# Optimization experiments

Measured on AMD Instinct MI355X. Metric: run time of the kernel, lower is better.

The kernel has to match this reference:

```python
import jax, jax.numpy as jnp
import numpy as np
from jax import lax
import math

N_QUBITS = 10
N_LAYERS = 4
PI = jnp.float32(math.pi)


def _c(x):
    return x.astype(jnp.complex64)


def rx_mat(t):
    c = _c(jnp.cos(0.5 * t)); s = _c(jnp.sin(0.5 * t))
    return jnp.stack([jnp.stack([c, -1j * s]), jnp.stack([-1j * s, c])])


def ry_mat(t):
    c = _c(jnp.cos(0.5 * t)); s = _c(jnp.sin(0.5 * t))
    return jnp.stack([jnp.stack([c, -s]), jnp.stack([s, c])])


def rz_mat(t):
    e0 = jnp.exp(_c(jnp.zeros_like(t)) - 0.5j * _c(t))
    e1 = jnp.exp(0.5j * _c(t))
    z = jnp.zeros_like(e0)
    return jnp.stack([jnp.stack([e0, z]), jnp.stack([z, e1])])


def apply_1q(psi, U, q):
    # psi: (2,)*n complex, apply 2x2 U on axis q
    psi = jnp.moveaxis(psi, q, 0)
    psi = jnp.tensordot(U, psi, axes=(1, 0))
    return jnp.moveaxis(psi, 0, q)


def apply_cnot(psi, ctrl, tgt):
    psi = jnp.moveaxis(psi, (ctrl, tgt), (0, 1))
    a00, a01, a10, a11 = psi[0, 0], psi[0, 1], psi[1, 0], psi[1, 1]
    psi = jnp.stack([jnp.stack([a00, a01]), jnp.stack([a11, a10])])
    return jnp.moveaxis(psi, (0, 1), (ctrl, tgt))


def vqc(state, weights):
    # state: (D,) float32 angles; weights: (layers, n, 3)
    n, L = N_QUBITS, N_LAYERS
    D = state.shape[0]
    psi = jnp.full((2,) * n, 2.0 ** (-n / 2.0), dtype=jnp.complex64)  # H^n |0>
    for layer in range(L):
        for q in range(n):
            ang = state[(layer * n + q) % D]
            psi = apply_1q(psi, rx_mat(ang), q)
            psi = apply_1q(psi, ry_mat(ang), q)
            psi = apply_1q(psi, rz_mat(weights[layer, q, 0]), q)
            psi = apply_1q(psi, ry_mat(weights[layer, q, 1]), q)
            psi = apply_1q(psi, rz_mat(weights[layer, q, 2]), q)
        for q in range(n - 1):
            psi = apply_cnot(psi, q, q + 1)
        psi = apply_cnot(psi, n - 1, 0)
    probs = jnp.real(psi * jnp.conj(psi))  # (2,)*n
    zdiag = jnp.array([1.0, -1.0], dtype=jnp.float32)
    exps = [jnp.sum(probs * zdiag.reshape((1,) * q + (2,) + (1,) * (n - q - 1)))
            for q in range(n)]
    return jnp.stack(exps)  # (n,)


def lstm_forward(x, W_ih, W_hh, b_ih, b_hh):
    # x: [B,T,Din]; PyTorch gate order: i, f, g, o
    B, T, _ = x.shape
    H = W_hh.shape[1]
    b = b_ih + b_hh

    def step(carry, xt):
        h, c = carry
        gates = xt @ W_ih.T + h @ W_hh.T + b
        i, f, g, o = jnp.split(gates, 4, axis=-1)
        i = jax.nn.sigmoid(i); f = jax.nn.sigmoid(f)
        g = jnp.tanh(g); o = jax.nn.sigmoid(o)
        c = f * c + i * g
        h = o * jnp.tanh(c)
        return (h, c), h

    h0 = jnp.zeros((B, H), x.dtype)
    c0 = jnp.zeros((B, H), x.dtype)
    _, hs = lax.scan(step, (h0, c0), jnp.swapaxes(x, 0, 1))
    return jnp.swapaxes(hs, 0, 1)  # [B,T,H]


def _forward(s, lstm_s, W_ih, W_hh, b_ih, b_hh, proj_W, proj_b,
             in_proj_W, in_proj_b, out_proj_W, out_proj_b,
             qweights, W1, b1, W2, b2):
    hs = lstm_forward(lstm_s, W_ih, W_hh, b_ih, b_hh)      # [B,T,H]
    lstm_last = hs[:, -1, :]                               # [B,H]
    state_full = jnp.concatenate([lstm_last, s], axis=1)   # [B,E]
    lstm_proj = hs @ proj_W.T + proj_b                     # [B,T,E]
    E = proj_W.shape[0]
    Wq, Wk, Wv = in_proj_W[:E], in_proj_W[E:2 * E], in_proj_W[2 * E:]
    bq, bk, bv = in_proj_b[:E], in_proj_b[E:2 * E], in_proj_b[2 * E:]
    q = state_full @ Wq.T + bq                             # [B,E] (1 query token)
    k = lstm_proj @ Wk.T + bk                              # [B,T,E]
    v = lstm_proj @ Wv.T + bv
    scale = 1.0 / jnp.sqrt(jnp.float32(E))                 # num_heads=1 -> head_dim=E
    attn = jax.nn.softmax(jnp.einsum('be,bte->bt', q, k) * scale, axis=-1)
    ctx = jnp.einsum('bt,bte->be', attn, v)
    attn_out = ctx @ out_proj_W.T + out_proj_b             # [B,E]
    merged_state = jnp.concatenate([attn_out, s], axis=1)  # [B,E+F]
    state_norm = jnp.tanh(merged_state) * PI
    qfeat = jax.vmap(lambda st: vqc(st, qweights))(state_norm)  # [B,n]
    merged = jnp.concatenate([merged_state, qfeat], axis=1)
    x = jax.nn.relu(merged @ W1.T + b1)
    return x @ W2.T + b2


def setup_inputs() -> dict:
    key = jax.random.key(0)
    ks = jax.random.split(key, 16)
    B, T = 512, 256
    Din, H, F = 128, 256, 64
    E = H + F          # 320 = state_dim
    Dm = E + F         # 384 = merged_state dim
    n_l1, n_act = 512, 8

    def g(k, shape, std):
        return (std * jax.random.normal(k, shape)).astype(jnp.float32)

    return {
        's': jax.random.normal(ks[0], (B, F), jnp.float32),
        'lstm_s': jax.random.normal(ks[1], (B, T, Din), jnp.float32),
        'W_ih': g(ks[2], (4 * H, Din), 0.05),
        'W_hh': g(ks[3], (4 * H, H), 0.05),
        'b_ih': jnp.zeros((4 * H,), jnp.float32),
        'b_hh': jnp.zeros((4 * H,), jnp.float32),
        'proj_W': g(ks[4], (E, H), 0.05),
        'proj_b': 0.1 * jnp.ones((E,), jnp.float32),
        'in_proj_W': g(ks[5], (3 * E, E), 0.05),
        'in_proj_b': jnp.zeros((3 * E,), jnp.float32),
        'out_proj_W': g(ks[6], (E, E), 0.05),
        'out_proj_b': jnp.zeros((E,), jnp.float32),
        'qweights': jax.random.uniform(ks[7], (N_LAYERS, N_QUBITS, 3), jnp.float32, 0.0, 2.0 * math.pi),
        'W1': g(ks[8], (n_l1, Dm + N_QUBITS), 0.05),
        'b1': 0.1 * jnp.ones((n_l1,), jnp.float32),
        'W2': g(ks[9], (n_act, n_l1), 0.05),
        'b2': 0.1 * jnp.ones((n_act,), jnp.float32),
    }


def reference(s, lstm_s, W_ih, W_hh, b_ih, b_hh, proj_W, proj_b,
              in_proj_W, in_proj_b, out_proj_W, out_proj_b,
              qweights, W1, b1, W2, b2):
    return _forward(s, lstm_s, W_ih, W_hh, b_ih, b_hh, proj_W, proj_b,
                    in_proj_W, in_proj_b, out_proj_W, out_proj_b,
                    qweights, W1, b1, W2, b2)
```

## Files before the change

### kernel.cpp

```cpp
#include <hip/hip_runtime.h>
#include <hip/hip_bf16.h>
#include <math.h>

typedef unsigned int u32;
typedef unsigned long long u64;
typedef unsigned short u16;
typedef __attribute__((ext_vector_type(8))) short short8;
typedef __attribute__((ext_vector_type(4))) float f32x4;
typedef __attribute__((ext_vector_type(4))) int v4i;

#define PI_F 3.14159265358979f
#define B_   512
#define T_   256
#define DIN  128
#define H_   256
#define G4   1024
#define F_   64
#define E_   320
#define DM   384
#define NL1  512
#define NACT 8
#define KMLP 394

__device__ v4i llvm_amdgcn_raw_buffer_load_v4i32(v4i rsrc, int voffset,
                                                 int soffset, int aux)
    __asm("llvm.amdgcn.raw.buffer.load.v4i32");
__device__ void llvm_amdgcn_raw_buffer_store_i32(int vdata, v4i rsrc,
                                                 int voffset, int soffset,
                                                 int aux)
    __asm("llvm.amdgcn.raw.buffer.store.i32");

__device__ __forceinline__ v4i make_srd(const void* p) {
  v4i r;
  r.x = (int)(u32)(u64)p;
  r.y = (int)(u32)((u64)p >> 32);
  r.z = (int)0xFFFFFFFFu;
  r.w = 0x00020000;
  return r;
}

__device__ __forceinline__ float b2f(u16 h) {
  union { u32 u; float f; } v; v.u = ((u32)h) << 16; return v.f;
}
__device__ __forceinline__ u16 f2b(float f) {
  union { float f; u32 u; } v; v.f = f;
  u32 r = (v.u + 0x7FFFu + ((v.u >> 16) & 1u)) >> 16;
  return (u16)r;
}
__device__ __forceinline__ float sigf(float x) { return 1.0f / (1.0f + __expf(-x)); }
__device__ __forceinline__ float tanhfast(float x) { return 2.0f / (1.0f + __expf(-2.0f * x)) - 1.0f; }
__device__ __forceinline__ float2 cmul(float2 a, float2 b) {
  return make_float2(a.x * b.x - a.y * b.y, a.x * b.y + a.y * b.x);
}
__device__ __forceinline__ float2 cadd(float2 a, float2 b) {
  return make_float2(a.x + b.x, a.y + b.y);
}

__global__ void k_prep1(const float* __restrict__ lstm_s,
                        const float* __restrict__ W_ih,
                        const float* __restrict__ W_hh,
                        const float* __restrict__ b_ih,
                        const float* __restrict__ b_hh,
                        const float* __restrict__ ipw,
                        const float* __restrict__ ipb,
                        const float* __restrict__ projb,
                        const float* __restrict__ qw,
                        const float* __restrict__ W1,
                        u16* __restrict__ xbf,
                        u16* __restrict__ hs,
                        u16* __restrict__ Wg,
                        float* __restrict__ bb,
                        float* __restrict__ W1t,
                        float* __restrict__ uw,
                        float* __restrict__ bkp,
                        float* __restrict__ bvp,
                        u32* __restrict__ cnt) {
  const int bid = blockIdx.x;
  const int tid = threadIdx.x;
  if (bid < 8192) {
    u32 u = (u32)bid * 256u + tid;
    u32 c8 = u & 15u, b = (u >> 4) & 511u, t = u >> 13;
    const float* src = lstm_s + ((size_t)b * T_ + t) * DIN + c8 * 8;
    union { u16 h[8]; uint4 v; } tmp;
#pragma unroll
    for (int i = 0; i < 8; ++i) tmp.h[i] = f2b(src[i]);
    *(uint4*)(xbf + ((size_t)t * B_ + b) * DIN + c8 * 8) = tmp.v;
  } else if (bid < 8384) {
    u32 u = (u32)(bid - 8192) * 256u + tid;
    u32 c8 = u % 48u, r = u / 48u;
    const float* src = (c8 < 16) ? (W_ih + (size_t)r * DIN + c8 * 8)
                                 : (W_hh + (size_t)r * H_ + (c8 - 16) * 8);
    union { u16 h[8]; uint4 v; } tmp;
#pragma unroll
    for (int i = 0; i < 8; ++i) tmp.h[i] = f2b(src[i]);
    *(uint4*)(Wg + (size_t)r * 384 + c8 * 8) = tmp.v;
  } else if (bid < 8448) {
    u32 u = (u32)(bid - 8384) * 256u + tid;
    ((uint4*)hs)[u] = make_uint4(0, 0, 0, 0);
  } else if (bid < 9236) {
    u32 u = (u32)(bid - 8448) * 256u + tid;
    u32 k = u / 512u, nn = u % 512u;
    W1t[u] = W1[(size_t)nn * KMLP + k];
  } else if (bid == 9236) {
    for (int i = tid; i < 1024; i += 256) bb[i] = b_ih[i] + b_hh[i];
    for (int i = tid; i < 1024; i += 256) cnt[i] = 0u;
    if (tid < 40) {
      float w0 = qw[tid * 3 + 0], w1 = qw[tid * 3 + 1], w2 = qw[tid * 3 + 2];
      float c0 = cosf(0.5f * w0), s0 = sinf(0.5f * w0);
      float c1 = cosf(0.5f * w1), s1 = sinf(0.5f * w1);
      float c2 = cosf(0.5f * w2), s2 = sinf(0.5f * w2);
      float2 e0m = make_float2(c0, -s0), e0p = make_float2(c0, s0);
      float2 e2m = make_float2(c2, -s2), e2p = make_float2(c2, s2);
      float2 t00 = make_float2(c1 * e0m.x, c1 * e0m.y);
      float2 t01 = make_float2(-s1 * e0p.x, -s1 * e0p.y);
      float2 t10 = make_float2(s1 * e0m.x, s1 * e0m.y);
      float2 t11 = make_float2(c1 * e0p.x, c1 * e0p.y);
      float2 u00 = cmul(e2m, t00), u01 = cmul(e2m, t01);
      float2 u10 = cmul(e2p, t10), u11 = cmul(e2p, t11);
      float* o = uw + tid * 8;
      o[0] = u00.x; o[1] = u00.y; o[2] = u01.x; o[3] = u01.y;
      o[4] = u10.x; o[5] = u10.y; o[6] = u11.x; o[7] = u11.y;
    }
  } else if (bid <= 9238) {
    int o = (bid - 9237) * 256 + tid;
    if (o < E_) {
      float acc = ipb[E_ + o];
      for (int e = 0; e < E_; ++e) acc += ipw[(size_t)(E_ + o) * E_ + e] * projb[e];
      bkp[o] = acc;
    }
  } else {
    int o = (bid - 9239) * 256 + tid;
    if (o < E_) {
      float acc = ipb[2 * E_ + o];
      for (int e = 0; e < E_; ++e) acc += ipw[(size_t)(2 * E_ + o) * E_ + e] * projb[e];
      bvp[o] = acc;
    }
  }
}

__global__ void k_prep2(const float* __restrict__ ipw, const float* __restrict__ projW,
                        float* __restrict__ Wkp, float* __restrict__ Wvp) {
  int bid = blockIdx.x, tid = threadIdx.x;
  int o = (bid < 320) ? bid : (bid - 320);
  const float* wrow = ipw + (size_t)((bid < 320 ? E_ : 2 * E_) + o) * E_;
  float acc = 0.f;
  for (int e = 0; e < E_; ++e) acc += wrow[e] * projW[(size_t)e * H_ + tid];
  (bid < 320 ? Wkp : Wvp)[(size_t)o * H_ + tid] = acc;
}

__global__ void k_prep3(const float* __restrict__ ipw, const float* __restrict__ ipb,
                        const float* __restrict__ opw, const float* __restrict__ opb,
                        const float* __restrict__ Wkp, const float* __restrict__ Wvp,
                        const float* __restrict__ bkp, const float* __restrict__ bvp,
                        float* __restrict__ WuT, float* __restrict__ bu,
                        float* __restrict__ wd, float* __restrict__ ddp,
                        float* __restrict__ Wovt, float* __restrict__ bov) {
  int bid = blockIdx.x, tid = threadIdx.x;
  if (bid < 320) {
    int e = bid;
    float acc = 0.f;
    for (int o = 0; o < E_; ++o) acc += Wkp[(size_t)o * H_ + tid] * ipw[(size_t)o * E_ + e];
    WuT[(size_t)e * H_ + tid] = acc;
  } else if (bid < 576) {
    int jj = bid - 320;
    for (int i = tid; i < E_; i += 256) {
      float acc = 0.f;
      for (int o = 0; o < E_; ++o) acc += opw[(size_t)i * E_ + o] * Wvp[(size_t)o * H_ + jj];
      Wovt[(size_t)jj * E_ + i] = acc;
    }
  } else {
    {
      float acc = 0.f;
      for (int o = 0; o < E_; ++o) acc += Wkp[(size_t)o * H_ + tid] * ipb[o];
      bu[tid] = acc;
    }
    for (int idx = tid; idx < E_; idx += 256) {
      float a1 = 0.f, a2 = opb[idx];
      for (int o = 0; o < E_; ++o) {
        a1 += ipw[(size_t)o * E_ + idx] * bkp[o];
        a2 += opw[(size_t)idx * E_ + o] * bvp[o];
      }
      wd[idx] = a1; bov[idx] = a2;
    }
    if (tid == 0) {
      float acc = 0.f;
      for (int o = 0; o < E_; ++o) acc += ipb[o] * bkp[o];
      ddp[0] = acc;
    }
  }
}

struct LstmArgs {
  const u16* xbf; u16* hs; const u16* Wg; const float* bb; u32* cnt;
};

__launch_bounds__(256, 1)
__global__ void k_lstm(LstmArgs A) {
  const int g   = blockIdx.x & 7;
  const int n   = blockIdx.x >> 3;
  const int tid = threadIdx.x;
  const int wid = tid >> 6, lane = tid & 63;
  __shared__ __align__(16) u16 Wl[32 * 392];

  for (int idx = tid; idx < 32 * 48; idx += 256) {
    int ln = idx / 48, c8 = idx % 48;
    int gr = (ln >> 3) * 256 + n * 8 + (ln & 7);
    *(uint4*)&Wl[ln * 392 + c8 * 8] = *(const uint4*)&A.Wg[(size_t)gr * 384 + c8 * 8];
  }
  const int j  = lane & 7;
  const int gc = n * 8 + j;
  const float bbi = A.bb[gc], bbf2 = A.bb[256 + gc];
  const float bbg = A.bb[512 + gc], bbo = A.bb[768 + gc];

  const int quad = lane >> 4;
  const int mrow = lane & 15;
  const int brow = g * 64 + wid * 16 + mrow;
  const int erow0 = g * 64 + wid * 16 + quad * 4;
  const bool hi = (lane & 8) != 0;
  float crs[4] = {0.f, 0.f, 0.f, 0.f};
  u32* mycnt = A.cnt + g * 64;
  u32 target = 0;

  const v4i hs_srd = make_srd(A.hs);
  const int hvoff = (brow * H_ + quad * 8) * 2;

  uint4 xc0, xc1, xc2, xc3, xn0, xn1, xn2, xn3;
  {
    const u16* xb = A.xbf + ((size_t)0 * B_ + brow) * DIN + quad * 8;
    xc0 = *(const uint4*)(xb + 0);
    xc1 = *(const uint4*)(xb + 32);
    xc2 = *(const uint4*)(xb + 64);
    xc3 = *(const uint4*)(xb + 96);
  }
  __syncthreads();

  for (int t = 0; t < T_; ++t) {
    const int hsoff = t * (B_ * H_ * 2);
    uint4 h0 = __builtin_bit_cast(uint4, llvm_amdgcn_raw_buffer_load_v4i32(hs_srd, hvoff +   0, hsoff, 17));
    uint4 h1 = __builtin_bit_cast(uint4, llvm_amdgcn_raw_buffer_load_v4i32(hs_srd, hvoff +  64, hsoff, 17));
    uint4 h2 = __builtin_bit_cast(uint4, llvm_amdgcn_raw_buffer_load_v4i32(hs_srd, hvoff + 128, hsoff, 17));
    uint4 h3 = __builtin_bit_cast(uint4, llvm_amdgcn_raw_buffer_load_v4i32(hs_srd, hvoff + 192, hsoff, 17));
    uint4 h4 = __builtin_bit_cast(uint4, llvm_amdgcn_raw_buffer_load_v4i32(hs_srd, hvoff + 256, hsoff, 17));
    uint4 h5 = __builtin_bit_cast(uint4, llvm_amdgcn_raw_buffer_load_v4i32(hs_srd, hvoff + 320, hsoff, 17));
    uint4 h6 = __builtin_bit_cast(uint4, llvm_amdgcn_raw_buffer_load_v4i32(hs_srd, hvoff + 384, hsoff, 17));
    uint4 h7 = __builtin_bit_cast(uint4, llvm_amdgcn_raw_buffer_load_v4i32(hs_srd, hvoff + 448, hsoff, 17));
    {
      const int tn = (t + 1 < T_) ? (t + 1) : t;
      const u16* xb = A.xbf + ((size_t)tn * B_ + brow) * DIN + quad * 8;
      xn0 = *(const uint4*)(xb + 0);
      xn1 = *(const uint4*)(xb + 32);
      xn2 = *(const uint4*)(xb + 64);
      xn3 = *(const uint4*)(xb + 96);
    }

    f32x4 acc0 = {0.f, 0.f, 0.f, 0.f}, acc1 = {0.f, 0.f, 0.f, 0.f};
#define MMSTEP(AV, KOFF)                                                          \
    {                                                                             \
      short8 av  = __builtin_bit_cast(short8, AV);                                \
      short8 bv0 = __builtin_bit_cast(short8,                                     \
          *(const uint4*)&Wl[mrow * 392 + (KOFF) + quad * 8]);                    \
      short8 bv1 = __builtin_bit_cast(short8,                                     \
          *(const uint4*)&Wl[(16 + mrow) * 392 + (KOFF) + quad * 8]);             \
      acc0 = __builtin_amdgcn_mfma_f32_16x16x32_bf16(av, bv0, acc0, 0, 0, 0);     \
      acc1 = __builtin_amdgcn_mfma_f32_16x16x32_bf16(av, bv1, acc1, 0, 0, 0);     \
    }
    MMSTEP(xc0, 0)   MMSTEP(xc1, 32)  MMSTEP(xc2, 64)  MMSTEP(xc3, 96)
    MMSTEP(h0, 128)  MMSTEP(h1, 160)  MMSTEP(h2, 192)  MMSTEP(h3, 224)
    MMSTEP(h4, 256)  MMSTEP(h5, 288)  MMSTEP(h6, 320)  MMSTEP(h7, 352)
#undef MMSTEP

    const int hsoff_o = (t + 1) * (B_ * H_ * 2);
#pragma unroll
    for (int r = 0; r < 4; ++r) {
      float x0 = acc0[r], x1v = acc1[r];
      float y0 = __shfl_xor(x0, 8, 64);
      float y1 = __shfl_xor(x1v, 8, 64);
      float iv = (hi ? y0 : x0) + bbi;
      float fv = (hi ? x0 : y0) + bbf2;
      float gv = (hi ? y1 : x1v) + bbg;
      float ov = (hi ? x1v : y1) + bbo;
      float cc = sigf(fv) * crs[r] + sigf(iv) * tanhfast(gv);
      crs[r] = cc;
      float hh = sigf(ov) * tanhfast(cc);
      float hh2 = __shfl_xor(hh, 1, 64);
      if (!hi && ((j & 1) == 0)) {
        u32 pk = (u32)f2b(hh) | ((u32)f2b(hh2) << 16);
        llvm_amdgcn_raw_buffer_store_i32((int)pk, hs_srd,
                                         ((erow0 + r) * H_ + gc) * 2, hsoff_o, 17);
      }
    }
    target += 32;
    if (t != T_ - 1) {
      __syncthreads();
      if (tid == 0) {
        __hip_atomic_fetch_add(mycnt, 1u, __ATOMIC_RELAXED, __HIP_MEMORY_SCOPE_AGENT);
        int guard = 0;
        while (__hip_atomic_load(mycnt, __ATOMIC_RELAXED, __HIP_MEMORY_SCOPE_AGENT) < target) {
          __builtin_amdgcn_s_sleep(1);
          if (++guard > (1 << 24)) break;
        }
      }
      __syncthreads();
      xc0 = xn0; xc1 = xn1; xc2 = xn2; xc3 = xn3;
    }
  }
}

__global__ void k_post(const u16* __restrict__ hs, const float* __restrict__ s,
                       const float* __restrict__ WuT, const float* __restrict__ bu,
                       const float* __restrict__ wd, const float* __restrict__ ddp,
                       const float* __restrict__ Wovt, const float* __restrict__ bov,
                       const float* __restrict__ uwg,
                       const float* __restrict__ W1t, const float* __restrict__ b1,
                       const float* __restrict__ W2, const float* __restrict__ b2,
                       float* __restrict__ out) {
  int b = blockIdx.x, tid = threadIdx.x;
  int wid = tid >> 6, lane = tid & 63;
  __shared__ float z[E_];
  __shared__ float red[256];
  __shared__ float ul_s[H_];
  __shared__ float sc[T_];
  __shared__ float wv_s[H_];
  __shared__ float mst_l[DM];
  __shared__ float dvec_s;
  __shared__ float2 psi[1024];
  __shared__ float ang[40];
  __shared__ float uwl[320];
  __shared__ float part[4][10];
  __shared__ float qf_s[10];
  __shared__ float mg[KMLP];
  __shared__ float x1[NL1];

  z[tid] = b2f(hs[((size_t)T_ * B_ + b) * H_ + tid]);
  if (tid < F_) z[H_ + tid] = s[(size_t)b * F_ + tid];
  __syncthreads();
  {
    float acc = bu[tid];
    for (int e = 0; e < E_; ++e) acc += WuT[(size_t)e * H_ + tid] * z[e];
    ul_s[tid] = acc;
    float p = 0.f;
    for (int e = tid; e < E_; e += 256) p += wd[e] * z[e];
    red[tid] = p;
    __syncthreads();
    for (int s2 = 128; s2 > 0; s2 >>= 1) {
      if (tid < s2) red[tid] += red[tid + s2];
      __syncthreads();
    }
    if (tid == 0) dvec_s = red[0] + ddp[0];
    __syncthreads();
  }

  {
    const float db = dvec_s;
    const float scale = 0.055901699437494745f;
    float4 ul = make_float4(ul_s[lane * 4], ul_s[lane * 4 + 1],
                            ul_s[lane * 4 + 2], ul_s[lane * 4 + 3]);
    for (int tt = 0; tt < 64; ++tt) {
      int t = wid * 64 + tt;
      u32 rw0 = ((const u32*)(hs + ((size_t)(t + 1) * B_ + b) * H_))[lane * 2];
      u32 rw1 = ((const u32*)(hs + ((size_t)(t + 1) * B_ + b) * H_))[lane * 2 + 1];
      union { u32 uu; float f; } f0, f1, f2, f3;
      f0.uu = rw0 << 16; f1.uu = rw0 & 0xFFFF0000u;
      f2.uu = rw1 << 16; f3.uu = rw1 & 0xFFFF0000u;
      float p = f0.f * ul.x + f1.f * ul.y + f2.f * ul.z + f3.f * ul.w;
#pragma unroll
      for (int off = 32; off > 0; off >>= 1) p += __shfl_xor(p, off, 64);
      if (lane == 0) sc[t] = (p + db) * scale;
    }
    __syncthreads();
    float v = sc[tid];
    red[tid] = v;
    __syncthreads();
    for (int s2 = 128; s2 > 0; s2 >>= 1) {
      if (tid < s2) red[tid] = fmaxf(red[tid], red[tid + s2]);
      __syncthreads();
    }
    float m = red[0];
    __syncthreads();
    float e = __expf(v - m);
    red[tid] = e;
    __syncthreads();
    for (int s2 = 128; s2 > 0; s2 >>= 1) {
      if (tid < s2) red[tid] += red[tid + s2];
      __syncthreads();
    }
    float inv = 1.f / red[0];
    __syncthreads();
    sc[tid] = e * inv;
    __syncthreads();
    float acc = 0.f;
#pragma unroll 8
    for (int t = 0; t < T_; ++t) {
      acc += sc[t] * b2f(hs[((size_t)(t + 1) * B_ + b) * H_ + tid]);
    }
    wv_s[tid] = acc;
    __syncthreads();
  }

  {
    for (int i = tid; i < E_; i += 256) {
      float acc = bov[i];
      for (int jj = 0; jj < H_; ++jj) acc += Wovt[(size_t)jj * E_ + i] * wv_s[jj];
      mst_l[i] = acc;
    }
    if (tid < F_) mst_l[E_ + tid] = s[(size_t)b * F_ + tid];
    __syncthreads();
  }

  {
    if (tid < 40) ang[tid] = tanhf(mst_l[tid]) * PI_F;
    uwl[tid] = uwg[tid];
    if (tid < 64) uwl[256 + tid] = uwg[256 + tid];
#pragma unroll
    for (int k = 0; k < 4; ++k) psi[tid + k * 256] = make_float2(0.03125f, 0.f);
    __syncthreads();
    for (int l = 0; l < 4; ++l) {
      for (int q = 0; q < 10; ++q) {
        int lq = l * 10 + q;
        float a = ang[lq];
        float ca = __cosf(0.5f * a), sa = __sinf(0.5f * a);
        float cs = ca * sa;
        float2 m00 = make_float2(ca * ca, sa * sa);
        float2 m01 = make_float2(-cs, -cs);
        float2 m10 = make_float2(cs, -cs);
        float2 m11 = make_float2(ca * ca, -sa * sa);
        const float* uwp = &uwl[lq * 8];
        float2 a00 = make_float2(uwp[0], uwp[1]), a01 = make_float2(uwp[2], uwp[3]);
        float2 a10 = make_float2(uwp[4], uwp[5]), a11 = make_float2(uwp[6], uwp[7]);
        float2 u00 = cadd(cmul(a00, m00), cmul(a01, m10));
        float2 u01 = cadd(cmul(a00, m01), cmul(a01, m11));
        float2 u10 = cadd(cmul(a10, m00), cmul(a11, m10));
        float2 u11 = cadd(cmul(a10, m01), cmul(a11, m11));
        int bp = 9 - q;
        __syncthreads();
#pragma unroll
        for (int k = 0; k < 2; ++k) {
          int p = tid + k * 256;
          int i0 = ((p >> bp) << (bp + 1)) | (p & ((1 << bp) - 1));
          int i1 = i0 | (1 << bp);
          float2 A0 = psi[i0], A1 = psi[i1];
          psi[i0] = cadd(cmul(u00, A0), cmul(u01, A1));
          psi[i1] = cadd(cmul(u10, A0), cmul(u11, A1));
        }
      }
      for (int q = 0; q < 9; ++q) {
        int lo = 8 - q;
        __syncthreads();
        int p = tid;
        int i0 = ((p >> lo) << (lo + 2)) | (2 << lo) | (p & ((1 << lo) - 1));
        int i1 = i0 | (1 << lo);
        float2 tmp = psi[i0]; psi[i0] = psi[i1]; psi[i1] = tmp;
      }
      __syncthreads();
      {
        int i0 = (tid << 1) | 1;
        int i1 = i0 | 512;
        float2 tmp = psi[i0]; psi[i0] = psi[i1]; psi[i1] = tmp;
      }
    }
    __syncthreads();
    float acc[10];
#pragma unroll
    for (int q = 0; q < 10; ++q) acc[q] = 0.f;
#pragma unroll
    for (int k = 0; k < 4; ++k) {
      int idx = tid + k * 256;
      float2 A = psi[idx];
      float pr = A.x * A.x + A.y * A.y;
#pragma unroll
      for (int q = 0; q < 10; ++q) acc[q] += ((idx >> (9 - q)) & 1) ? -pr : pr;
    }
#pragma unroll
    for (int q = 0; q < 10; ++q) {
      float vq = acc[q];
#pragma unroll
      for (int off = 32; off > 0; off >>= 1) vq += __shfl_xor(vq, off, 64);
      if (lane == 0) part[wid][q] = vq;
    }
    __syncthreads();
    if (tid < 10) qf_s[tid] = part[0][tid] + part[1][tid] + part[2][tid] + part[3][tid];
  }

  {
    for (int i = tid; i < DM; i += 256) mg[i] = mst_l[i];
    if (tid < 10) mg[DM + tid] = qf_s[tid];
    __syncthreads();
#pragma unroll
    for (int hh = 0; hh < 2; ++hh) {
      int nn = tid + hh * 256;
      float acc = b1[nn];
#pragma unroll 4
      for (int k = 0; k < KMLP; ++k) acc += W1t[(size_t)k * NL1 + nn] * mg[k];
      x1[nn] = fmaxf(acc, 0.f);
    }
    __syncthreads();
    int a = tid >> 5, l32 = tid & 31;
    float p = 0.f;
    for (int k = l32; k < NL1; k += 32) p += x1[k] * W2[(size_t)a * NL1 + k];
    red[tid] = p;
    __syncthreads();
    if (tid < 8) {
      float acc = b2[tid];
#pragma unroll
      for (int i = 0; i < 32; ++i) acc += red[tid * 32 + i];
      out[(size_t)b * NACT + tid] = acc;
    }
  }
}

extern "C" void kernel_launch(void* const* d_in, const int* in_sizes, int n_in,
                              void* d_out, int out_size, void* d_ws, size_t ws_size,
                              hipStream_t stream) {
  const float* s      = (const float*)d_in[0];
  const float* lstm_s = (const float*)d_in[1];
  const float* W_ih   = (const float*)d_in[2];
  const float* W_hh   = (const float*)d_in[3];
  const float* b_ih   = (const float*)d_in[4];
  const float* b_hh   = (const float*)d_in[5];
  const float* projW  = (const float*)d_in[6];
  const float* projb  = (const float*)d_in[7];
  const float* ipw    = (const float*)d_in[8];
  const float* ipb    = (const float*)d_in[9];
  const float* opw    = (const float*)d_in[10];
  const float* opb    = (const float*)d_in[11];
  const float* qw     = (const float*)d_in[12];
  const float* W1     = (const float*)d_in[13];
  const float* b1     = (const float*)d_in[14];
  const float* W2     = (const float*)d_in[15];
  const float* b2     = (const float*)d_in[16];
  float* out = (float*)d_out;

  char* wsb = (char*)d_ws;
  size_t off = 0;
  auto alloc = [&](size_t bytes) -> void* {
    void* p = wsb + off;
    off = (off + bytes + 255) & ~(size_t)255;
    return p;
  };
  u16*  xbf  = (u16*)alloc((size_t)T_ * B_ * DIN * 2);
  u16*  hs   = (u16*)alloc((size_t)(T_ + 1) * B_ * H_ * 2);
  u16*  Wg   = (u16*)alloc((size_t)G4 * 384 * 2);
  float* bb  = (float*)alloc(G4 * 4);
  float* Wkp = (float*)alloc((size_t)E_ * H_ * 4);
  float* Wvp = (float*)alloc((size_t)E_ * H_ * 4);
  float* bkp = (float*)alloc(E_ * 4);
  float* bvp = (float*)alloc(E_ * 4);
  float* WuT = (float*)alloc((size_t)E_ * H_ * 4);
  float* bu  = (float*)alloc(H_ * 4);
  float* wd  = (float*)alloc(E_ * 4);
  float* ddp = (float*)alloc(256);
  float* Wovt= (float*)alloc((size_t)H_ * E_ * 4);
  float* bov = (float*)alloc(E_ * 4);
  float* uw  = (float*)alloc(40 * 8 * 4);
  float* W1t = (float*)alloc((size_t)KMLP * NL1 * 4);
  u32*  cnt  = (u32*)alloc(1024 * 4);
  (void)ws_size; (void)in_sizes; (void)n_in; (void)out_size;

  hipLaunchKernelGGL(k_prep1, dim3(9241), dim3(256), 0, stream,
                     lstm_s, W_ih, W_hh, b_ih, b_hh, ipw, ipb, projb, qw, W1,
                     xbf, hs, Wg, bb, W1t, uw, bkp, bvp, cnt);
  hipLaunchKernelGGL(k_prep2, dim3(640), dim3(256), 0, stream, ipw, projW, Wkp, Wvp);
  hipLaunchKernelGGL(k_prep3, dim3(577), dim3(256), 0, stream,
                     ipw, ipb, opw, opb, Wkp, Wvp, bkp, bvp, WuT, bu, wd, ddp, Wovt, bov);

  LstmArgs la;
  la.xbf = xbf; la.hs = hs; la.Wg = Wg; la.bb = bb; la.cnt = cnt;
  void* kargs[] = { (void*)&la };
  hipError_t ce = hipLaunchCooperativeKernel(reinterpret_cast<const void*>(&k_lstm),
                                             dim3(256), dim3(256), kargs, 0, stream);
  if (ce != hipSuccess) {
    hipLaunchKernelGGL(k_lstm, dim3(256), dim3(256), 0, stream, la);
  }

  hipLaunchKernelGGL(k_post, dim3(512), dim3(256), 0, stream,
                     hs, s, WuT, bu, wd, ddp, Wovt, bov, uw, W1t, b1, W2, b2, out);
}
```

Before: 1.295 ms.

## Fold attention weight precompute into extra LSTM blocks and split post accumulators

```diff
diff --git a/kernel.cpp b/kernel.cpp
--- a/kernel.cpp
+++ b/kernel.cpp
@@ -25,10 +25,17 @@
 __device__ v4i llvm_amdgcn_raw_buffer_load_v4i32(v4i rsrc, int voffset,
                                                  int soffset, int aux)
     __asm("llvm.amdgcn.raw.buffer.load.v4i32");
+__device__ float llvm_amdgcn_raw_buffer_load_f32(v4i rsrc, int voffset,
+                                                 int soffset, int aux)
+    __asm("llvm.amdgcn.raw.buffer.load.f32");
 __device__ void llvm_amdgcn_raw_buffer_store_i32(int vdata, v4i rsrc,
                                                  int voffset, int soffset,
                                                  int aux)
     __asm("llvm.amdgcn.raw.buffer.store.i32");
+__device__ void llvm_amdgcn_raw_buffer_store_f32(float vdata, v4i rsrc,
+                                                 int voffset, int soffset,
+                                                 int aux)
+    __asm("llvm.amdgcn.raw.buffer.store.f32");
 
 __device__ __forceinline__ v4i make_srd(const void* p) {
   v4i r;
@@ -138,69 +145,101 @@
   }
 }
 
-__global__ void k_prep2(const float* __restrict__ ipw, const float* __restrict__ projW,
-                        float* __restrict__ Wkp, float* __restrict__ Wvp) {
-  int bid = blockIdx.x, tid = threadIdx.x;
-  int o = (bid < 320) ? bid : (bid - 320);
-  const float* wrow = ipw + (size_t)((bid < 320 ? E_ : 2 * E_) + o) * E_;
-  float acc = 0.f;
-  for (int e = 0; e < E_; ++e) acc += wrow[e] * projW[(size_t)e * H_ + tid];
-  (bid < 320 ? Wkp : Wvp)[(size_t)o * H_ + tid] = acc;
-}
-
-__global__ void k_prep3(const float* __restrict__ ipw, const float* __restrict__ ipb,
-                        const float* __restrict__ opw, const float* __restrict__ opb,
-                        const float* __restrict__ Wkp, const float* __restrict__ Wvp,
-                        const float* __restrict__ bkp, const float* __restrict__ bvp,
-                        float* __restrict__ WuT, float* __restrict__ bu,
-                        float* __restrict__ wd, float* __restrict__ ddp,
-                        float* __restrict__ Wovt, float* __restrict__ bov) {
-  int bid = blockIdx.x, tid = threadIdx.x;
-  if (bid < 320) {
-    int e = bid;
-    float acc = 0.f;
-    for (int o = 0; o < E_; ++o) acc += Wkp[(size_t)o * H_ + tid] * ipw[(size_t)o * E_ + e];
-    WuT[(size_t)e * H_ + tid] = acc;
-  } else if (bid < 576) {
-    int jj = bid - 320;
-    for (int i = tid; i < E_; i += 256) {
-      float acc = 0.f;
-      for (int o = 0; o < E_; ++o) acc += opw[(size_t)i * E_ + o] * Wvp[(size_t)o * H_ + jj];
-      Wovt[(size_t)jj * E_ + i] = acc;
-    }
-  } else {
-    {
-      float acc = 0.f;
-      for (int o = 0; o < E_; ++o) acc += Wkp[(size_t)o * H_ + tid] * ipb[o];
-      bu[tid] = acc;
-    }
-    for (int idx = tid; idx < E_; idx += 256) {
-      float a1 = 0.f, a2 = opb[idx];
-      for (int o = 0; o < E_; ++o) {
-        a1 += ipw[(size_t)o * E_ + idx] * bkp[o];
-        a2 += opw[(size_t)idx * E_ + o] * bvp[o];
-      }
-      wd[idx] = a1; bov[idx] = a2;
-    }
-    if (tid == 0) {
-      float acc = 0.f;
-      for (int o = 0; o < E_; ++o) acc += ipb[o] * bkp[o];
-      ddp[0] = acc;
-    }
-  }
-}
-
 struct LstmArgs {
   const u16* xbf; u16* hs; const u16* Wg; const float* bb; u32* cnt;
+  const float* ipw; const float* ipb; const float* projW;
+  const float* opw; const float* opb;
+  const float* bkp; const float* bvp;
+  float* Wkp; float* Wvp;
+  float* WuT; float* bu; float* wd; float* ddp; float* Wovt; float* bov;
 };
 
 __launch_bounds__(256, 1)
 __global__ void k_lstm(LstmArgs A) {
+  const int tid = threadIdx.x;
+  __shared__ __align__(16) u16 Wl[32 * 392];
+
+  if (blockIdx.x >= 256) {
+    const int p = blockIdx.x - 256;
+    const v4i kp_srd = make_srd(A.Wkp);
+    const v4i vp_srd = make_srd(A.Wvp);
+    for (int o = p; o < E_; o += 256) {
+      const float* rk = A.ipw + (size_t)(E_ + o) * E_;
+      const float* rv = A.ipw + (size_t)(2 * E_ + o) * E_;
+      float ak = 0.f, av = 0.f;
+#pragma unroll 4
+      for (int e = 0; e < E_; ++e) {
+        float pw = A.projW[(size_t)e * H_ + tid];
+        ak += rk[e] * pw;
+        av += rv[e] * pw;
+      }
+      llvm_amdgcn_raw_buffer_store_f32(ak, kp_srd, (o * H_ + tid) * 4, 0, 17);
+      llvm_amdgcn_raw_buffer_store_f32(av, vp_srd, (o * H_ + tid) * 4, 0, 17);
+    }
+    __syncthreads();
+    if (tid == 0) {
+      u32* pc = A.cnt + 768;
+      __hip_atomic_fetch_add(pc, 1u, __ATOMIC_RELAXED, __HIP_MEMORY_SCOPE_AGENT);
+      int guard = 0;
+      while (__hip_atomic_load(pc, __ATOMIC_RELAXED, __HIP_MEMORY_SCOPE_AGENT) < 256u) {
+        __builtin_amdgcn_s_sleep(1);
+        if (++guard > (1 << 24)) break;
+      }
+    }
+    __syncthreads();
+    for (int e = p; e < E_; e += 256) {
+      float acc = 0.f;
+#pragma unroll 4
+      for (int o = 0; o < E_; ++o) {
+        float kv = llvm_amdgcn_raw_buffer_load_f32(kp_srd, (o * H_ + tid) * 4, 0, 17);
+        acc += kv * A.ipw[(size_t)o * E_ + e];
+      }
+      A.WuT[(size_t)e * H_ + tid] = acc;
+    }
+    {
+      const int jj = p;
+      for (int i = tid; i < E_; i += 256) {
+        const float* wo = A.opw + (size_t)i * E_;
+        float acc = 0.f;
+#pragma unroll 4
+        for (int o = 0; o < E_; ++o) {
+          float vv = llvm_amdgcn_raw_buffer_load_f32(vp_srd, (o * H_ + jj) * 4, 0, 17);
+          acc += wo[o] * vv;
+        }
+        A.Wovt[(size_t)jj * E_ + i] = acc;
+      }
+    }
+    if (p == 0) {
+      {
+        float acc = 0.f;
+#pragma unroll 4
+        for (int o = 0; o < E_; ++o) {
+          float kv = llvm_amdgcn_raw_buffer_load_f32(kp_srd, (o * H_ + tid) * 4, 0, 17);
+          acc += kv * A.ipb[o];
+        }
+        A.bu[tid] = acc;
+      }
+      for (int idx = tid; idx < E_; idx += 256) {
+        float a1 = 0.f, a2 = A.opb[idx];
+#pragma unroll 4
+        for (int o = 0; o < E_; ++o) {
+          a1 += A.ipw[(size_t)o * E_ + idx] * A.bkp[o];
+          a2 += A.opw[(size_t)idx * E_ + o] * A.bvp[o];
+        }
+        A.wd[idx] = a1; A.bov[idx] = a2;
+      }
+      if (tid == 0) {
+        float acc = 0.f;
+        for (int o = 0; o < E_; ++o) acc += A.ipb[o] * A.bkp[o];
+        A.ddp[0] = acc;
+      }
+    }
+    return;
+  }
+
   const int g   = blockIdx.x & 7;
   const int n   = blockIdx.x >> 3;
-  const int tid = threadIdx.x;
   const int wid = tid >> 6, lane = tid & 63;
-  __shared__ __align__(16) u16 Wl[32 * 392];
 
   for (int idx = tid; idx < 32 * 48; idx += 256) {
     int ln = idx / 48, c8 = idx % 48;
@@ -335,9 +374,13 @@
   if (tid < F_) z[H_ + tid] = s[(size_t)b * F_ + tid];
   __syncthreads();
   {
-    float acc = bu[tid];
-    for (int e = 0; e < E_; ++e) acc += WuT[(size_t)e * H_ + tid] * z[e];
-    ul_s[tid] = acc;
+    float a0 = bu[tid], a1 = 0.f;
+#pragma unroll 8
+    for (int e = 0; e < 160; ++e) {
+      a0 += WuT[(size_t)e * H_ + tid] * z[e];
+      a1 += WuT[(size_t)(e + 160) * H_ + tid] * z[e + 160];
+    }
+    ul_s[tid] = a0 + a1;
     float p = 0.f;
     for (int e = tid; e < E_; e += 256) p += wd[e] * z[e];
     red[tid] = p;
@@ -388,20 +431,25 @@
     __syncthreads();
     sc[tid] = e * inv;
     __syncthreads();
-    float acc = 0.f;
+    float a0 = 0.f, a1 = 0.f;
 #pragma unroll 8
-    for (int t = 0; t < T_; ++t) {
-      acc += sc[t] * b2f(hs[((size_t)(t + 1) * B_ + b) * H_ + tid]);
-    }
-    wv_s[tid] = acc;
+    for (int t = 0; t < 128; ++t) {
+      a0 += sc[t]       * b2f(hs[((size_t)(t + 1) * B_ + b) * H_ + tid]);
+      a1 += sc[t + 128] * b2f(hs[((size_t)(t + 129) * B_ + b) * H_ + tid]);
+    }
+    wv_s[tid] = a0 + a1;
     __syncthreads();
   }
 
   {
     for (int i = tid; i < E_; i += 256) {
-      float acc = bov[i];
-      for (int jj = 0; jj < H_; ++jj) acc += Wovt[(size_t)jj * E_ + i] * wv_s[jj];
-      mst_l[i] = acc;
+      float a0 = bov[i], a1 = 0.f;
+#pragma unroll 8
+      for (int jj = 0; jj < 128; ++jj) {
+        a0 += Wovt[(size_t)jj * E_ + i] * wv_s[jj];
+        a1 += Wovt[(size_t)(jj + 128) * E_ + i] * wv_s[jj + 128];
+      }
+      mst_l[i] = a0 + a1;
     }
     if (tid < F_) mst_l[E_ + tid] = s[(size_t)b * F_ + tid];
     __syncthreads();
@@ -485,14 +533,15 @@
     for (int i = tid; i < DM; i += 256) mg[i] = mst_l[i];
     if (tid < 10) mg[DM + tid] = qf_s[tid];
     __syncthreads();
-#pragma unroll
-    for (int hh = 0; hh < 2; ++hh) {
-      int nn = tid + hh * 256;
-      float acc = b1[nn];
-#pragma unroll 4
-      for (int k = 0; k < KMLP; ++k) acc += W1t[(size_t)k * NL1 + nn] * mg[k];
-      x1[nn] = fmaxf(acc, 0.f);
-    }
+    float a0 = b1[tid], a1 = b1[tid + 256];
+#pragma unroll 8
+    for (int k = 0; k < KMLP; ++k) {
+      float m = mg[k];
+      a0 += W1t[(size_t)k * NL1 + tid] * m;
+      a1 += W1t[(size_t)k * NL1 + tid + 256] * m;
+    }
+    x1[tid] = fmaxf(a0, 0.f);
+    x1[tid + 256] = fmaxf(a1, 0.f);
     __syncthreads();
     int a = tid >> 5, l32 = tid & 31;
     float p = 0.f;
@@ -559,17 +608,17 @@
   hipLaunchKernelGGL(k_prep1, dim3(9241), dim3(256), 0, stream,
                      lstm_s, W_ih, W_hh, b_ih, b_hh, ipw, ipb, projb, qw, W1,
                      xbf, hs, Wg, bb, W1t, uw, bkp, bvp, cnt);
-  hipLaunchKernelGGL(k_prep2, dim3(640), dim3(256), 0, stream, ipw, projW, Wkp, Wvp);
-  hipLaunchKernelGGL(k_prep3, dim3(577), dim3(256), 0, stream,
-                     ipw, ipb, opw, opb, Wkp, Wvp, bkp, bvp, WuT, bu, wd, ddp, Wovt, bov);
 
   LstmArgs la;
   la.xbf = xbf; la.hs = hs; la.Wg = Wg; la.bb = bb; la.cnt = cnt;
+  la.ipw = ipw; la.ipb = ipb; la.projW = projW; la.opw = opw; la.opb = opb;
+  la.bkp = bkp; la.bvp = bvp; la.Wkp = Wkp; la.Wvp = Wvp;
+  la.WuT = WuT; la.bu = bu; la.wd = wd; la.ddp = ddp; la.Wovt = Wovt; la.bov = bov;
   void* kargs[] = { (void*)&la };
   hipError_t ce = hipLaunchCooperativeKernel(reinterpret_cast<const void*>(&k_lstm),
-                                             dim3(256), dim3(256), kargs, 0, stream);
+                                             dim3(512), dim3(256), kargs, 0, stream);
   if (ce != hipSuccess) {
-    hipLaunchKernelGGL(k_lstm, dim3(256), dim3(256), 0, stream, la);
+    hipLaunchKernelGGL(k_lstm, dim3(512), dim3(256), 0, stream, la);
   }
 
   hipLaunchKernelGGL(k_post, dim3(512), dim3(256), 0, stream,
```

Result: faster. 1.206 ms (-6.8%).
